# Kernel tuning notes

Measured on AMD Instinct MI355X. Metric: run time of the kernel, lower is better.

## Reference

```python
import jax, jax.numpy as jnp
import numpy as np

B, T, F, E = 256, 256, 8, 128
H = 2 * E  # hidden_dim = 2*embedding_dim = 256
NL = 5     # num_layers per LSTM stack


def setup_inputs() -> dict:
    key = jax.random.key(0)
    ks = jax.random.split(key, 9)
    s1 = 1.0 / np.sqrt(H)
    s2 = 1.0 / np.sqrt(E)
    u = lambda k, shape, s: jax.random.uniform(k, shape, jnp.float32, -s, s)
    return {
        "x": jax.random.normal(ks[0], (B, T, F), jnp.float32),
        # stack 1: input F -> hidden H, 5 layers. b = b_ih + b_hh combined.
        "w_ih0_1": u(ks[1], (4 * H, F), s1),
        "w_ihr_1": u(ks[2], (NL - 1, 4 * H, H), s1),
        "w_hh_1": u(ks[3], (NL, 4 * H, H), s1),
        "b_1": u(ks[4], (NL, 4 * H), s1),
        # stack 2: input H -> hidden E, 5 layers
        "w_ih0_2": u(ks[5], (4 * E, H), s2),
        "w_ihr_2": u(ks[6], (NL - 1, 4 * E, E), s2),
        "w_hh_2": u(ks[7], (NL, 4 * E, E), s2),
        "b_2": u(ks[8], (NL, 4 * E), s2),
    }


def _lstm_layer(x, w_ih, w_hh, b):
    """x: [B,T,D] -> (outputs [B,T,Hd], final hidden [B,Hd]). PyTorch gate order i,f,g,o."""
    Hd = w_hh.shape[-1]
    # precompute input contribution for all timesteps (the big GEMM)
    xg = jnp.einsum('btd,gd->tbg', x, w_ih) + b  # [T,B,4Hd]
    h0 = jnp.zeros((x.shape[0], Hd), x.dtype)

    def step(carry, xt):
        h, c = carry
        g = xt + h @ w_hh.T
        i, f, gg, o = jnp.split(g, 4, axis=-1)
        c = jax.nn.sigmoid(f) * c + jax.nn.sigmoid(i) * jnp.tanh(gg)
        h = jax.nn.sigmoid(o) * jnp.tanh(c)
        return (h, c), h

    (h, _), hs = jax.lax.scan(step, (h0, h0), xg)
    return jnp.swapaxes(hs, 0, 1), h


def _stack(x, w_ih0, w_ihr, w_hh, b):
    y, h = _lstm_layer(x, w_ih0, w_hh[0], b[0])
    for l in range(1, w_hh.shape[0]):
        y, h = _lstm_layer(y, w_ihr[l - 1], w_hh[l], b[l])
    return y, h


def reference(x, w_ih0_1, w_ihr_1, w_hh_1, b_1, w_ih0_2, w_ihr_2, w_hh_2, b_2):
    x = x.reshape(x.shape[0], T, F)
    y, _ = _stack(x, w_ih0_1, w_ihr_1, w_hh_1, b_1)   # [B,T,H]
    _, h = _stack(y, w_ih0_2, w_ihr_2, w_hh_2, b_2)   # h: [B,E] last layer final hidden
    return h
```

## Files before the change

### kernel.cpp

```cpp
#include <hip/hip_runtime.h>
#include <math.h>

typedef unsigned short u16;
typedef unsigned int   u32;
typedef unsigned long long u64;
typedef __bf16 bf16x8 __attribute__((ext_vector_type(8)));
typedef float  f32x4  __attribute__((ext_vector_type(4)));

#define BB 256
#define TT 256
#define HD 256
#define ED 128
#define NSTEPS 265

#define H_U32   (10 * 2 * BB * HD)
#define CTR_OFF H_U32
#define CTR_U32 512
#define XP_OFF  (H_U32 + CTR_U32)
#define XP_U32  (BB * TT * 8)
#define WT_OFF  (XP_OFF + XP_U32)

__constant__ size_t g_woff[10] = {0ul,589824ul,1638400ul,2686976ul,3735552ul,
                                  4784128ul,5177344ul,5439488ul,5701632ul,5963776ul};
__constant__ int g_cb[11] = {0,73728,204800,335872,466944,598016,
                             647168,679936,712704,745472,778240};

__device__ __forceinline__ u16 f2bf_hi(float f) {
    u32 u = __float_as_uint(f);
    u32 r = (u + 0x7FFFu + ((u >> 16) & 1u)) >> 16;
    return (u16)r;
}
__device__ __forceinline__ float bf2f(u16 h) { return __uint_as_float(((u32)h) << 16); }
__device__ __forceinline__ float sigmoidf_(float v) { return 1.0f / (1.0f + expf(-v)); }

__global__ __launch_bounds__(256) void zero_state(u32* wsd) {
    const int n = XP_OFF;
    for (int i = blockIdx.x * blockDim.x + threadIdx.x; i < n; i += gridDim.x * blockDim.x)
        wsd[i] = 0u;
}

__global__ __launch_bounds__(256) void conv_x(const float* __restrict__ x, u32* __restrict__ wsd) {
    u32* xp = wsd + XP_OFF;
    for (int i = blockIdx.x * blockDim.x + threadIdx.x; i < XP_U32; i += gridDim.x * blockDim.x) {
        float v = x[i];
        u16 hi = f2bf_hi(v);
        u16 lo = f2bf_hi(v - bf2f(hi));
        xp[i] = (u32)hi | ((u32)lo << 16);
    }
}

__global__ __launch_bounds__(256) void conv_all(
    const float* __restrict__ w_ih0_1, const float* __restrict__ w_ihr_1,
    const float* __restrict__ w_hh_1,
    const float* __restrict__ w_ih0_2, const float* __restrict__ w_ihr_2,
    const float* __restrict__ w_hh_2,
    u32* __restrict__ wsd)
{
    __bf16* dst0 = (__bf16*)(wsd + WT_OFF);
    const int nch = 778240;
    for (int ci = blockIdx.x * blockDim.x + threadIdx.x; ci < nch;
         ci += gridDim.x * blockDim.x) {
        int l = 0;
        while (ci >= g_cb[l + 1]) ++l;
        int di = ci - g_cb[l];

        const int hd  = (l < 5) ? 256 : 128;
        const int din = (l == 0) ? 32 : ((l < 6) ? 256 : 128);
        const int xw  = (l == 0) ? 8 : din;
        const int Kp  = din + hd;
        const int nk  = Kp >> 5;

        const float *wih, *whh; int wihld, whhld;
        if (l == 0)      { wih = w_ih0_1;                                whh = w_hh_1;
                           wihld = 8;   whhld = 256; }
        else if (l < 5)  { wih = w_ihr_1 + (size_t)(l - 1) * 1024 * 256; whh = w_hh_1 + (size_t)l * 1024 * 256;
                           wihld = 256; whhld = 256; }
        else if (l == 5) { wih = w_ih0_2;                                whh = w_hh_2;
                           wihld = 256; whhld = 128; }
        else             { wih = w_ihr_2 + (size_t)(l - 6) * 512 * 128;  whh = w_hh_2 + (size_t)(l - 5) * 512 * 128;
                           wihld = 128; whhld = 128; }

        int lane = di & 63;
        int rem  = di >> 6;
        int kt   = rem % nk;
        int rem2 = rem / nk;
        int p    = rem2 & 1;
        int g    = (rem2 >> 1) & 3;
        int jt   = rem2 >> 3;
        int r15  = lane & 15, kq = lane >> 4;
        int row  = g * hd + jt * 16 + r15;

        bf16x8 o8;
        #pragma unroll
        for (int e = 0; e < 8; ++e) {
            int k = kt * 32 + kq * 8 + e;
            float v = 0.0f;
            if (k < xw) v = wih[(size_t)row * wihld + k];
            else if (k >= din && k < Kp) v = whh[(size_t)row * whhld + (k - din)];
            __bf16 h = (__bf16)v;
            o8[e] = p ? (__bf16)(v - (float)h) : h;
        }
        *(bf16x8*)(dst0 + g_woff[l] + (size_t)di * 8) = o8;
    }
}

__device__ __forceinline__ void unpack8(const uint4& a, const uint4& b, bf16x8& bh, bf16x8& bl) {
    union { u32 u[4]; bf16x8 v; } H, L;
    H.u[0] = (a.x & 0xFFFFu) | (a.y << 16);
    H.u[1] = (a.z & 0xFFFFu) | (a.w << 16);
    H.u[2] = (b.x & 0xFFFFu) | (b.y << 16);
    H.u[3] = (b.z & 0xFFFFu) | (b.w << 16);
    L.u[0] = (a.x >> 16) | (a.y & 0xFFFF0000u);
    L.u[1] = (a.z >> 16) | (a.w & 0xFFFF0000u);
    L.u[2] = (b.x >> 16) | (b.y & 0xFFFF0000u);
    L.u[3] = (b.z >> 16) | (b.w & 0xFFFF0000u);
    bh = H.v; bl = L.v;
}

template<int NKI, int NKT, bool ISL0>
__device__ void run_persist(int l, int bid, int xcd, int jt, int bt, int hd,
    const float* __restrict__ bias, u32* __restrict__ hbuf, u32* __restrict__ ctr,
    const u32* __restrict__ xp, float* __restrict__ out, const u16* __restrict__ A_sh)
{
    constexpr int DIN = NKI * 32;
    constexpr int RD  = (NKT < 8) ? NKT : 8;

    const int tid  = threadIdx.x;
    const int lane = tid & 63;
    const int wv   = tid >> 6;
    const int r15  = lane & 15;
    const int kq   = lane >> 4;
    const int brow = bt * 128 + wv * 16 + r15;
    const int j0   = jt * 16 + kq * 4;

    float bgr[4][4];
    #pragma unroll
    for (int g = 0; g < 4; ++g) {
        float4 v = *(const float4*)&bias[g * hd + j0];
        bgr[g][0] = v.x; bgr[g][1] = v.y; bgr[g][2] = v.z; bgr[g][3] = v.w;
    }

    int offH[4], offL[4];
    #pragma unroll
    for (int g = 0; g < 4; ++g) {
        offH[g] = (g * 2)     * NKT * 512 + lane * 8;
        offL[g] = (g * 2 + 1) * NKT * 512 + lane * 8;
    }

    float4 cv = make_float4(0.f, 0.f, 0.f, 0.f);
    const int lm = (l > 0) ? (l - 1) : 0;

    for (int w = 0; w < NSTEPS; ++w) {
        const int t = w - l;
        if (t >= 0 && t < TT) {
            const u32* hin   = hbuf + ((size_t)lm * 2 + (t & 1)) * (BB * HD);
            const u32* hprev = hbuf + ((size_t)l * 2 + ((t & 1) ^ 1)) * (BB * HD);
            u32*       hout  = hbuf + ((size_t)l * 2 + (t & 1)) * (BB * HD);

            auto ldB = [&](int kt, uint4& A, uint4& B) {
                if constexpr (ISL0) {
                    if (kt == 0) {
                        if (kq == 0) {
                            const uint4* p = (const uint4*)(xp + ((size_t)brow * TT + t) * 8);
                            A = p[0]; B = p[1];
                        } else { A = make_uint4(0,0,0,0); B = make_uint4(0,0,0,0); }
                    } else {
                        const u32* p = hprev + (size_t)brow * HD + (kt * 32 - 32) + kq * 8;
                        A = *(const uint4*)p; B = *(const uint4*)(p + 4);
                    }
                } else {
                    const int k0 = kt * 32 + kq * 8;
                    const u32* p = (kt < NKI) ? (hin + (size_t)brow * HD + k0)
                                              : (hprev + (size_t)brow * HD + (k0 - DIN));
                    A = *(const uint4*)p; B = *(const uint4*)(p + 4);
                }
            };

            f32x4 acc0 = {0.f,0.f,0.f,0.f}, acc1 = {0.f,0.f,0.f,0.f};
            f32x4 acc2 = {0.f,0.f,0.f,0.f}, acc3 = {0.f,0.f,0.f,0.f};

            uint4 rA[RD], rB[RD];
            #pragma unroll
            for (int i = 0; i < RD; ++i) ldB(i, rA[i], rB[i]);

            #pragma unroll
            for (int kt = 0; kt < NKT; ++kt) {
                bf16x8 bh, bl;
                unpack8(rA[kt % RD], rB[kt % RD], bh, bl);
                if (kt + RD < NKT) ldB(kt + RD, rA[kt % RD], rB[kt % RD]);

                const int kof = kt * 512;
                bf16x8 a0h = *(const bf16x8*)&A_sh[offH[0] + kof];
                bf16x8 a1h = *(const bf16x8*)&A_sh[offH[1] + kof];
                bf16x8 a2h = *(const bf16x8*)&A_sh[offH[2] + kof];
                bf16x8 a3h = *(const bf16x8*)&A_sh[offH[3] + kof];
                bf16x8 a0l = *(const bf16x8*)&A_sh[offL[0] + kof];
                bf16x8 a1l = *(const bf16x8*)&A_sh[offL[1] + kof];
                bf16x8 a2l = *(const bf16x8*)&A_sh[offL[2] + kof];
                bf16x8 a3l = *(const bf16x8*)&A_sh[offL[3] + kof];

                acc0 = __builtin_amdgcn_mfma_f32_16x16x32_bf16(a0h, bh, acc0, 0, 0, 0);
                acc1 = __builtin_amdgcn_mfma_f32_16x16x32_bf16(a1h, bh, acc1, 0, 0, 0);
                acc2 = __builtin_amdgcn_mfma_f32_16x16x32_bf16(a2h, bh, acc2, 0, 0, 0);
                acc3 = __builtin_amdgcn_mfma_f32_16x16x32_bf16(a3h, bh, acc3, 0, 0, 0);
                acc0 = __builtin_amdgcn_mfma_f32_16x16x32_bf16(a0h, bl, acc0, 0, 0, 0);
                acc1 = __builtin_amdgcn_mfma_f32_16x16x32_bf16(a1h, bl, acc1, 0, 0, 0);
                acc2 = __builtin_amdgcn_mfma_f32_16x16x32_bf16(a2h, bl, acc2, 0, 0, 0);
                acc3 = __builtin_amdgcn_mfma_f32_16x16x32_bf16(a3h, bl, acc3, 0, 0, 0);
                acc0 = __builtin_amdgcn_mfma_f32_16x16x32_bf16(a0l, bh, acc0, 0, 0, 0);
                acc1 = __builtin_amdgcn_mfma_f32_16x16x32_bf16(a1l, bh, acc1, 0, 0, 0);
                acc2 = __builtin_amdgcn_mfma_f32_16x16x32_bf16(a2l, bh, acc2, 0, 0, 0);
                acc3 = __builtin_amdgcn_mfma_f32_16x16x32_bf16(a3l, bh, acc3, 0, 0, 0);
            }

            float4 hv;
            {
                float i_, f_, g_, o_;
                i_ = sigmoidf_(acc0[0] + bgr[0][0]); f_ = sigmoidf_(acc1[0] + bgr[1][0]);
                g_ = tanhf   (acc2[0] + bgr[2][0]); o_ = sigmoidf_(acc3[0] + bgr[3][0]);
                cv.x = fmaf(f_, cv.x, i_ * g_); hv.x = o_ * tanhf(cv.x);
                i_ = sigmoidf_(acc0[1] + bgr[0][1]); f_ = sigmoidf_(acc1[1] + bgr[1][1]);
                g_ = tanhf   (acc2[1] + bgr[2][1]); o_ = sigmoidf_(acc3[1] + bgr[3][1]);
                cv.y = fmaf(f_, cv.y, i_ * g_); hv.y = o_ * tanhf(cv.y);
                i_ = sigmoidf_(acc0[2] + bgr[0][2]); f_ = sigmoidf_(acc1[2] + bgr[1][2]);
                g_ = tanhf   (acc2[2] + bgr[2][2]); o_ = sigmoidf_(acc3[2] + bgr[3][2]);
                cv.z = fmaf(f_, cv.z, i_ * g_); hv.z = o_ * tanhf(cv.z);
                i_ = sigmoidf_(acc0[3] + bgr[0][3]); f_ = sigmoidf_(acc1[3] + bgr[1][3]);
                g_ = tanhf   (acc2[3] + bgr[2][3]); o_ = sigmoidf_(acc3[3] + bgr[3][3]);
                cv.w = fmaf(f_, cv.w, i_ * g_); hv.w = o_ * tanhf(cv.w);
            }

            u32 pk0, pk1, pk2, pk3;
            {
                u16 h0 = f2bf_hi(hv.x); pk0 = (u32)h0 | ((u32)f2bf_hi(hv.x - bf2f(h0)) << 16);
                u16 h1 = f2bf_hi(hv.y); pk1 = (u32)h1 | ((u32)f2bf_hi(hv.y - bf2f(h1)) << 16);
                u16 h2 = f2bf_hi(hv.z); pk2 = (u32)h2 | ((u32)f2bf_hi(hv.z - bf2f(h2)) << 16);
                u16 h3 = f2bf_hi(hv.w); pk3 = (u32)h3 | ((u32)f2bf_hi(hv.w - bf2f(h3)) << 16);
            }
            u64* hp = (u64*)(hout + (size_t)brow * HD + j0);
            __hip_atomic_store(hp + 0, (u64)pk0 | ((u64)pk1 << 32), __ATOMIC_RELAXED, __HIP_MEMORY_SCOPE_AGENT);
            __hip_atomic_store(hp + 1, (u64)pk2 | ((u64)pk3 << 32), __ATOMIC_RELAXED, __HIP_MEMORY_SCOPE_AGENT);

            if (l == 9 && t == TT - 1)
                *(float4*)&out[(size_t)brow * ED + j0] = hv;
        }

        __syncthreads();
        if (tid == 0) {
            __hip_atomic_fetch_add(&ctr[xcd * 32], 1u,
                                   __ATOMIC_RELAXED, __HIP_MEMORY_SCOPE_AGENT);
            const u32 w1 = (u32)(w + 1);
            if (bid == 0) {
                for (int it = 0; it < (1 << 22); ++it) {
                    bool ok = true;
                    #pragma unroll
                    for (int r = 0; r < 8; ++r) {
                        u32 tgt = ((r == 7) ? 16u : 32u) * w1;
                        ok &= (__hip_atomic_load(&ctr[r * 32], __ATOMIC_RELAXED,
                                                 __HIP_MEMORY_SCOPE_AGENT) >= tgt);
                    }
                    if (ok) break;
                    __builtin_amdgcn_s_sleep(1);
                }
                __hip_atomic_store(&ctr[256], w1, __ATOMIC_RELAXED, __HIP_MEMORY_SCOPE_AGENT);
            } else {
                for (int it = 0; it < (1 << 22); ++it) {
                    if (__hip_atomic_load(&ctr[256], __ATOMIC_RELAXED,
                                          __HIP_MEMORY_SCOPE_AGENT) >= w1) break;
                    __builtin_amdgcn_s_sleep(1);
                }
            }
            __builtin_amdgcn_fence(__ATOMIC_ACQUIRE, "agent");
        }
        __syncthreads();
    }
}

__global__ __launch_bounds__(512, 2) void lstm_persist(
    const float* __restrict__ b_1, const float* __restrict__ b_2,
    u32* __restrict__ wsd, float* __restrict__ out)
{
    __shared__ __align__(16) u16 A_sh[65536];

    const int bid = blockIdx.x;
    const int xcd = bid & 7, slot = bid >> 3;
    int l, jt, bt;
    if (xcd < 5)      { l = xcd;               bt = slot >> 4;        jt = slot & 15; }
    else if (xcd == 5){ l = 5 + (slot >> 4);   bt = (slot >> 3) & 1;  jt = slot & 7; }
    else if (xcd == 6){ l = 7 + (slot >> 4);   bt = (slot >> 3) & 1;  jt = slot & 7; }
    else              { if (slot >= 16) return; l = 9; bt = slot >> 3; jt = slot & 7; }

    const int hd  = (l < 5) ? 256 : 128;
    const int din = (l == 0) ? 32 : ((l < 6) ? 256 : 128);
    const int nk  = (din + hd) >> 5;
    const float* bias = (l < 5) ? (b_1 + l * 1024) : (b_2 + (l - 5) * 512);

    u32* hbuf = wsd;
    u32* ctr  = wsd + CTR_OFF;
    const u32* xp = wsd + XP_OFF;
    const u16* wt = (const u16*)(wsd + WT_OFF);

    {
        const uint4* src = (const uint4*)(wt + g_woff[l] + (size_t)jt * 8 * nk * 512);
        uint4* dst = (uint4*)A_sh;
        const int n4 = nk * 512;
        for (int i = threadIdx.x; i < n4; i += 512) dst[i] = src[i];
    }
    __syncthreads();

    if (l == 0)
        run_persist<1, 9, true >(l, bid, xcd, jt, bt, hd, bias, hbuf, ctr, xp, out, A_sh);
    else if (l < 5)
        run_persist<8, 16, false>(l, bid, xcd, jt, bt, hd, bias, hbuf, ctr, xp, out, A_sh);
    else if (l == 5)
        run_persist<8, 12, false>(l, bid, xcd, jt, bt, hd, bias, hbuf, ctr, xp, out, A_sh);
    else
        run_persist<4, 8, false>(l, bid, xcd, jt, bt, hd, bias, hbuf, ctr, xp, out, A_sh);
}

extern "C" void kernel_launch(void* const* d_in, const int* in_sizes, int n_in,
                              void* d_out, int out_size, void* d_ws, size_t ws_size,
                              hipStream_t stream) {
    const float* x       = (const float*)d_in[0];
    const float* w_ih0_1 = (const float*)d_in[1];
    const float* w_ihr_1 = (const float*)d_in[2];
    const float* w_hh_1  = (const float*)d_in[3];
    const float* b_1     = (const float*)d_in[4];
    const float* w_ih0_2 = (const float*)d_in[5];
    const float* w_ihr_2 = (const float*)d_in[6];
    const float* w_hh_2  = (const float*)d_in[7];
    const float* b_2     = (const float*)d_in[8];
    u32*   wsd = (u32*)d_ws;
    float* out = (float*)d_out;

    hipLaunchKernelGGL(zero_state, dim3(1024), dim3(256), 0, stream, wsd);
    hipLaunchKernelGGL(conv_all, dim3(1024), dim3(256), 0, stream,
                       w_ih0_1, w_ihr_1, w_hh_1, w_ih0_2, w_ihr_2, w_hh_2, wsd);
    hipLaunchKernelGGL(conv_x, dim3(256), dim3(256), 0, stream, x, wsd);
    hipLaunchKernelGGL(lstm_persist, dim3(256), dim3(512), 0, stream,
                       b_1, b_2, wsd, out);
}
```

Baseline: 3.286 ms.

## Switch recurrent GEMM to 32x32x16 MFMA with gate-interleaved weight layout

Replaces the four 16x16x32 MFMA accumulators per wave with a single 32x32x16 MFMA accumulator, where the 32 output rows interleave the four gates across 8 hidden units. The weight pre-pack and the LDS slice layout are reorganised to match, and waves are split by batch group and hidden half. This cuts LDS A-fragment loads per MFMA and uses the larger MFMA shape, but doubles the K-step count and changes how often the h buffer is loaded, which may raise latency on the serial recurrence path.

Result: slower. 5.104 ms (+55.3%).

```diff
diff --git a/kernel.cpp b/kernel.cpp
--- a/kernel.cpp
+++ b/kernel.cpp
@@ -5,7 +5,7 @@
 typedef unsigned int   u32;
 typedef unsigned long long u64;
 typedef __bf16 bf16x8 __attribute__((ext_vector_type(8)));
-typedef float  f32x4  __attribute__((ext_vector_type(4)));
+typedef float  f32x16 __attribute__((ext_vector_type(16)));
 
 #define BB 256
 #define TT 256
@@ -68,7 +68,7 @@
         const int din = (l == 0) ? 32 : ((l < 6) ? 256 : 128);
         const int xw  = (l == 0) ? 8 : din;
         const int Kp  = din + hd;
-        const int nk  = Kp >> 5;
+        const int NK2 = Kp >> 4;
 
         const float *wih, *whh; int wihld, whhld;
         if (l == 0)      { wih = w_ih0_1;                                whh = w_hh_1;
@@ -82,18 +82,20 @@
 
         int lane = di & 63;
         int rem  = di >> 6;
-        int kt   = rem % nk;
-        int rem2 = rem / nk;
+        int s    = rem % NK2;
+        int rem2 = rem / NK2;
         int p    = rem2 & 1;
-        int g    = (rem2 >> 1) & 3;
-        int jt   = rem2 >> 3;
-        int r15  = lane & 15, kq = lane >> 4;
-        int row  = g * hd + jt * 16 + r15;
+        int jh   = (rem2 >> 1) & 1;
+        int jt   = rem2 >> 2;
+        int r31  = lane & 31;
+        int gate = r31 >> 3, jl = r31 & 7;
+        int kh   = (lane >> 5) * 8;
+        int row  = gate * hd + jt * 16 + jh * 8 + jl;
 
         bf16x8 o8;
         #pragma unroll
         for (int e = 0; e < 8; ++e) {
-            int k = kt * 32 + kq * 8 + e;
+            int k = s * 16 + kh + e;
             float v = 0.0f;
             if (k < xw) v = wih[(size_t)row * wihld + k];
             else if (k >= din && k < Kp) v = whh[(size_t)row * whhld + (k - din)];
@@ -122,29 +124,28 @@
     const float* __restrict__ bias, u32* __restrict__ hbuf, u32* __restrict__ ctr,
     const u32* __restrict__ xp, float* __restrict__ out, const u16* __restrict__ A_sh)
 {
+    constexpr int NK2 = NKT * 2;
     constexpr int DIN = NKI * 32;
-    constexpr int RD  = (NKT < 8) ? NKT : 8;
-
-    const int tid  = threadIdx.x;
-    const int lane = tid & 63;
-    const int wv   = tid >> 6;
-    const int r15  = lane & 15;
-    const int kq   = lane >> 4;
-    const int brow = bt * 128 + wv * 16 + r15;
-    const int j0   = jt * 16 + kq * 4;
-
-    float bgr[4][4];
+    constexpr int RS  = (NK2 < 8) ? NK2 : 8;
+
+    const int tid   = threadIdx.x;
+    const int lane  = tid & 63;
+    const int wv    = tid >> 6;
+    const int bg    = wv >> 1;
+    const int jh    = wv & 1;
+    const int r31   = lane & 31;
+    const int kh    = (lane >> 5) * 8;
+    const int b     = bt * 128 + bg * 32 + r31;
+    const int jbase = jt * 16 + jh * 8 + (lane >> 5) * 4;
+
+    const int hiBase = ((jh * 2 + 0) * NK2) * 512 + lane * 8;
+    const int loBase = ((jh * 2 + 1) * NK2) * 512 + lane * 8;
+
+    float bias_r[4][4];
     #pragma unroll
     for (int g = 0; g < 4; ++g) {
-        float4 v = *(const float4*)&bias[g * hd + j0];
-        bgr[g][0] = v.x; bgr[g][1] = v.y; bgr[g][2] = v.z; bgr[g][3] = v.w;
-    }
-
-    int offH[4], offL[4];
-    #pragma unroll
-    for (int g = 0; g < 4; ++g) {
-        offH[g] = (g * 2)     * NKT * 512 + lane * 8;
-        offL[g] = (g * 2 + 1) * NKT * 512 + lane * 8;
+        float4 v = *(const float4*)&bias[g * hd + jbase];
+        bias_r[g][0] = v.x; bias_r[g][1] = v.y; bias_r[g][2] = v.z; bias_r[g][3] = v.w;
     }
 
     float4 cv = make_float4(0.f, 0.f, 0.f, 0.f);
@@ -157,76 +158,63 @@
             const u32* hprev = hbuf + ((size_t)l * 2 + ((t & 1) ^ 1)) * (BB * HD);
             u32*       hout  = hbuf + ((size_t)l * 2 + (t & 1)) * (BB * HD);
 
-            auto ldB = [&](int kt, uint4& A, uint4& B) {
+            auto ldB = [&](int s, uint4& qa, uint4& qb) {
                 if constexpr (ISL0) {
-                    if (kt == 0) {
-                        if (kq == 0) {
-                            const uint4* p = (const uint4*)(xp + ((size_t)brow * TT + t) * 8);
-                            A = p[0]; B = p[1];
-                        } else { A = make_uint4(0,0,0,0); B = make_uint4(0,0,0,0); }
+                    if (s == 0) {
+                        if (lane < 32) {
+                            const uint4* p = (const uint4*)(xp + ((size_t)b * TT + t) * 8);
+                            qa = p[0]; qb = p[1];
+                        } else { qa = make_uint4(0,0,0,0); qb = make_uint4(0,0,0,0); }
+                    } else if (s == 1) {
+                        qa = make_uint4(0,0,0,0); qb = make_uint4(0,0,0,0);
                     } else {
-                        const u32* p = hprev + (size_t)brow * HD + (kt * 32 - 32) + kq * 8;
-                        A = *(const uint4*)p; B = *(const uint4*)(p + 4);
+                        const u32* p = hprev + (size_t)b * HD + (s * 16 + kh - 32);
+                        qa = *(const uint4*)p; qb = *(const uint4*)(p + 4);
                     }
                 } else {
-                    const int k0 = kt * 32 + kq * 8;
-                    const u32* p = (kt < NKI) ? (hin + (size_t)brow * HD + k0)
-                                              : (hprev + (size_t)brow * HD + (k0 - DIN));
-                    A = *(const uint4*)p; B = *(const uint4*)(p + 4);
+                    const int k0 = s * 16 + kh;
+                    const u32* p = (k0 < DIN) ? (hin + (size_t)b * HD + k0)
+                                              : (hprev + (size_t)b * HD + (k0 - DIN));
+                    qa = *(const uint4*)p; qb = *(const uint4*)(p + 4);
                 }
             };
 
-            f32x4 acc0 = {0.f,0.f,0.f,0.f}, acc1 = {0.f,0.f,0.f,0.f};
-            f32x4 acc2 = {0.f,0.f,0.f,0.f}, acc3 = {0.f,0.f,0.f,0.f};
-
-            uint4 rA[RD], rB[RD];
+            f32x16 acc;
             #pragma unroll
-            for (int i = 0; i < RD; ++i) ldB(i, rA[i], rB[i]);
-
+            for (int i = 0; i < 16; ++i) acc[i] = 0.f;
+
+            uint4 ra[RS], rb[RS];
             #pragma unroll
-            for (int kt = 0; kt < NKT; ++kt) {
+            for (int i = 0; i < RS; ++i) ldB(i, ra[i], rb[i]);
+
+            #pragma unroll
+            for (int s = 0; s < NK2; ++s) {
                 bf16x8 bh, bl;
-                unpack8(rA[kt % RD], rB[kt % RD], bh, bl);
-                if (kt + RD < NKT) ldB(kt + RD, rA[kt % RD], rB[kt % RD]);
-
-                const int kof = kt * 512;
-                bf16x8 a0h = *(const bf16x8*)&A_sh[offH[0] + kof];
-                bf16x8 a1h = *(const bf16x8*)&A_sh[offH[1] + kof];
-                bf16x8 a2h = *(const bf16x8*)&A_sh[offH[2] + kof];
-                bf16x8 a3h = *(const bf16x8*)&A_sh[offH[3] + kof];
-                bf16x8 a0l = *(const bf16x8*)&A_sh[offL[0] + kof];
-                bf16x8 a1l = *(const bf16x8*)&A_sh[offL[1] + kof];
-                bf16x8 a2l = *(const bf16x8*)&A_sh[offL[2] + kof];
-                bf16x8 a3l = *(const bf16x8*)&A_sh[offL[3] + kof];
-
-                acc0 = __builtin_amdgcn_mfma_f32_16x16x32_bf16(a0h, bh, acc0, 0, 0, 0);
-                acc1 = __builtin_amdgcn_mfma_f32_16x16x32_bf16(a1h, bh, acc1, 0, 0, 0);
-                acc2 = __builtin_amdgcn_mfma_f32_16x16x32_bf16(a2h, bh, acc2, 0, 0, 0);
-                acc3 = __builtin_amdgcn_mfma_f32_16x16x32_bf16(a3h, bh, acc3, 0, 0, 0);
-                acc0 = __builtin_amdgcn_mfma_f32_16x16x32_bf16(a0h, bl, acc0, 0, 0, 0);
-                acc1 = __builtin_amdgcn_mfma_f32_16x16x32_bf16(a1h, bl, acc1, 0, 0, 0);
-                acc2 = __builtin_amdgcn_mfma_f32_16x16x32_bf16(a2h, bl, acc2, 0, 0, 0);
-                acc3 = __builtin_amdgcn_mfma_f32_16x16x32_bf16(a3h, bl, acc3, 0, 0, 0);
-                acc0 = __builtin_amdgcn_mfma_f32_16x16x32_bf16(a0l, bh, acc0, 0, 0, 0);
-                acc1 = __builtin_amdgcn_mfma_f32_16x16x32_bf16(a1l, bh, acc1, 0, 0, 0);
-                acc2 = __builtin_amdgcn_mfma_f32_16x16x32_bf16(a2l, bh, acc2, 0, 0, 0);
-                acc3 = __builtin_amdgcn_mfma_f32_16x16x32_bf16(a3l, bh, acc3, 0, 0, 0);
+                unpack8(ra[s % RS], rb[s % RS], bh, bl);
+                if (s + RS < NK2) ldB(s + RS, ra[s % RS], rb[s % RS]);
+
+                bf16x8 ah = *(const bf16x8*)&A_sh[hiBase + s * 512];
+                bf16x8 al = *(const bf16x8*)&A_sh[loBase + s * 512];
+
+                acc = __builtin_amdgcn_mfma_f32_32x32x16_bf16(ah, bh, acc, 0, 0, 0);
+                acc = __builtin_amdgcn_mfma_f32_32x32x16_bf16(ah, bl, acc, 0, 0, 0);
+                acc = __builtin_amdgcn_mfma_f32_32x32x16_bf16(al, bh, acc, 0, 0, 0);
             }
 
             float4 hv;
             {
                 float i_, f_, g_, o_;
-                i_ = sigmoidf_(acc0[0] + bgr[0][0]); f_ = sigmoidf_(acc1[0] + bgr[1][0]);
-                g_ = tanhf   (acc2[0] + bgr[2][0]); o_ = sigmoidf_(acc3[0] + bgr[3][0]);
+                i_ = sigmoidf_(acc[0]  + bias_r[0][0]); f_ = sigmoidf_(acc[4]  + bias_r[1][0]);
+                g_ = tanhf   (acc[8]  + bias_r[2][0]); o_ = sigmoidf_(acc[12] + bias_r[3][0]);
                 cv.x = fmaf(f_, cv.x, i_ * g_); hv.x = o_ * tanhf(cv.x);
-                i_ = sigmoidf_(acc0[1] + bgr[0][1]); f_ = sigmoidf_(acc1[1] + bgr[1][1]);
-                g_ = tanhf   (acc2[1] + bgr[2][1]); o_ = sigmoidf_(acc3[1] + bgr[3][1]);
+                i_ = sigmoidf_(acc[1]  + bias_r[0][1]); f_ = sigmoidf_(acc[5]  + bias_r[1][1]);
+                g_ = tanhf   (acc[9]  + bias_r[2][1]); o_ = sigmoidf_(acc[13] + bias_r[3][1]);
                 cv.y = fmaf(f_, cv.y, i_ * g_); hv.y = o_ * tanhf(cv.y);
-                i_ = sigmoidf_(acc0[2] + bgr[0][2]); f_ = sigmoidf_(acc1[2] + bgr[1][2]);
-                g_ = tanhf   (acc2[2] + bgr[2][2]); o_ = sigmoidf_(acc3[2] + bgr[3][2]);
+                i_ = sigmoidf_(acc[2]  + bias_r[0][2]); f_ = sigmoidf_(acc[6]  + bias_r[1][2]);
+                g_ = tanhf   (acc[10] + bias_r[2][2]); o_ = sigmoidf_(acc[14] + bias_r[3][2]);
                 cv.z = fmaf(f_, cv.z, i_ * g_); hv.z = o_ * tanhf(cv.z);
-                i_ = sigmoidf_(acc0[3] + bgr[0][3]); f_ = sigmoidf_(acc1[3] + bgr[1][3]);
-                g_ = tanhf   (acc2[3] + bgr[2][3]); o_ = sigmoidf_(acc3[3] + bgr[3][3]);
+                i_ = sigmoidf_(acc[3]  + bias_r[0][3]); f_ = sigmoidf_(acc[7]  + bias_r[1][3]);
+                g_ = tanhf   (acc[11] + bias_r[2][3]); o_ = sigmoidf_(acc[15] + bias_r[3][3]);
                 cv.w = fmaf(f_, cv.w, i_ * g_); hv.w = o_ * tanhf(cv.w);
             }
 
@@ -237,12 +225,12 @@
                 u16 h2 = f2bf_hi(hv.z); pk2 = (u32)h2 | ((u32)f2bf_hi(hv.z - bf2f(h2)) << 16);
                 u16 h3 = f2bf_hi(hv.w); pk3 = (u32)h3 | ((u32)f2bf_hi(hv.w - bf2f(h3)) << 16);
             }
-            u64* hp = (u64*)(hout + (size_t)brow * HD + j0);
+            u64* hp = (u64*)(hout + (size_t)b * HD + jbase);
             __hip_atomic_store(hp + 0, (u64)pk0 | ((u64)pk1 << 32), __ATOMIC_RELAXED, __HIP_MEMORY_SCOPE_AGENT);
             __hip_atomic_store(hp + 1, (u64)pk2 | ((u64)pk3 << 32), __ATOMIC_RELAXED, __HIP_MEMORY_SCOPE_AGENT);
 
             if (l == 9 && t == TT - 1)
-                *(float4*)&out[(size_t)brow * ED + j0] = hv;
+                *(float4*)&out[(size_t)b * ED + jbase] = hv;
         }
 
         __syncthreads();
@@ -292,7 +280,7 @@
 
     const int hd  = (l < 5) ? 256 : 128;
     const int din = (l == 0) ? 32 : ((l < 6) ? 256 : 128);
-    const int nk  = (din + hd) >> 5;
+    const int NK2 = (din + hd) >> 4;
     const float* bias = (l < 5) ? (b_1 + l * 1024) : (b_2 + (l - 5) * 512);
 
     u32* hbuf = wsd;
@@ -301,9 +289,9 @@
     const u16* wt = (const u16*)(wsd + WT_OFF);
 
     {
-        const uint4* src = (const uint4*)(wt + g_woff[l] + (size_t)jt * 8 * nk * 512);
+        const uint4* src = (const uint4*)(wt + g_woff[l] + (size_t)jt * 4 * NK2 * 512);
         uint4* dst = (uint4*)A_sh;
-        const int n4 = nk * 512;
+        const int n4 = NK2 * 256;
         for (int i = threadIdx.x; i < n4; i += 512) dst[i] = src[i];
     }
     __syncthreads();
```

## Retile LSTM step MFMA to 2x2 per-wave tiles with gate-interleaved weight rows

Applied to the files above, without the earlier changes.

Weight rows are re-laid out so each 16-row MFMA tile interleaves the four gates for four hidden units. Each wave now computes a 2x2 block: two weight tiles (hidden halves) by two batch tiles. This halves the LDS weight-fragment reads per MFMA and lets the gate nonlinearities run lane-locally from one accumulator. In exchange, each wave loads two batch rows of h, the prefetch depth drops from 8 to 4, and output stores become scattered 32-bit atomics instead of 64-bit vector stores.

After: 5.194 ms. 58.1% more time.

```diff
diff --git a/kernel.cpp b/kernel.cpp
--- a/kernel.cpp
+++ b/kernel.cpp
@@ -85,15 +85,17 @@
         int kt   = rem % nk;
         int rem2 = rem / nk;
         int p    = rem2 & 1;
-        int g    = (rem2 >> 1) & 3;
+        int mt   = (rem2 >> 1) & 1;
+        int jh   = (rem2 >> 2) & 1;
         int jt   = rem2 >> 3;
-        int r15  = lane & 15, kq = lane >> 4;
-        int row  = g * hd + jt * 16 + r15;
+        int r15  = lane & 15, kqc = lane >> 4;
+        int jloc = r15 >> 2, gate = r15 & 3;
+        int row  = gate * hd + jt * 16 + jh * 8 + mt * 4 + jloc;
 
         bf16x8 o8;
         #pragma unroll
         for (int e = 0; e < 8; ++e) {
-            int k = kt * 32 + kq * 8 + e;
+            int k = kt * 32 + kqc * 8 + e;
             float v = 0.0f;
             if (k < xw) v = wih[(size_t)row * wihld + k];
             else if (k >= din && k < Kp) v = whh[(size_t)row * whhld + (k - din)];
@@ -123,31 +125,31 @@
     const u32* __restrict__ xp, float* __restrict__ out, const u16* __restrict__ A_sh)
 {
     constexpr int DIN = NKI * 32;
-    constexpr int RD  = (NKT < 8) ? NKT : 8;
+    constexpr int RS  = (NKT < 4) ? NKT : 4;
 
     const int tid  = threadIdx.x;
     const int lane = tid & 63;
     const int wv   = tid >> 6;
+    const int bq   = wv >> 1;
+    const int jh   = wv & 1;
     const int r15  = lane & 15;
-    const int kq   = lane >> 4;
-    const int brow = bt * 128 + wv * 16 + r15;
-    const int j0   = jt * 16 + kq * 4;
-
-    float bgr[4][4];
+    const int kqc  = lane >> 4;
+    const int b0r  = bt * 128 + bq * 32 + r15;
+    const int jm0  = jt * 16 + jh * 8 + kqc;
+
+    const int hiB0 = ((jh * 4 + 0) * NKT) * 512 + lane * 8;
+    const int loB0 = ((jh * 4 + 1) * NKT) * 512 + lane * 8;
+    const int hiB1 = ((jh * 4 + 2) * NKT) * 512 + lane * 8;
+    const int loB1 = ((jh * 4 + 3) * NKT) * 512 + lane * 8;
+
+    float bias_r[2][4];
     #pragma unroll
-    for (int g = 0; g < 4; ++g) {
-        float4 v = *(const float4*)&bias[g * hd + j0];
-        bgr[g][0] = v.x; bgr[g][1] = v.y; bgr[g][2] = v.z; bgr[g][3] = v.w;
-    }
-
-    int offH[4], offL[4];
-    #pragma unroll
-    for (int g = 0; g < 4; ++g) {
-        offH[g] = (g * 2)     * NKT * 512 + lane * 8;
-        offL[g] = (g * 2 + 1) * NKT * 512 + lane * 8;
-    }
-
-    float4 cv = make_float4(0.f, 0.f, 0.f, 0.f);
+    for (int mt = 0; mt < 2; ++mt)
+        #pragma unroll
+        for (int g = 0; g < 4; ++g)
+            bias_r[mt][g] = bias[g * hd + jm0 + mt * 4];
+
+    f32x4 cv = {0.f, 0.f, 0.f, 0.f};
     const int lm = (l > 0) ? (l - 1) : 0;
 
     for (int w = 0; w < NSTEPS; ++w) {
@@ -157,92 +159,89 @@
             const u32* hprev = hbuf + ((size_t)l * 2 + ((t & 1) ^ 1)) * (BB * HD);
             u32*       hout  = hbuf + ((size_t)l * 2 + (t & 1)) * (BB * HD);
 
-            auto ldB = [&](int kt, uint4& A, uint4& B) {
+            auto ldB = [&](int kt, uint4& a0, uint4& b0q, uint4& a1, uint4& b1q) {
                 if constexpr (ISL0) {
                     if (kt == 0) {
-                        if (kq == 0) {
-                            const uint4* p = (const uint4*)(xp + ((size_t)brow * TT + t) * 8);
-                            A = p[0]; B = p[1];
-                        } else { A = make_uint4(0,0,0,0); B = make_uint4(0,0,0,0); }
+                        if (kqc == 0) {
+                            const uint4* p0 = (const uint4*)(xp + ((size_t)b0r * TT + t) * 8);
+                            const uint4* p1 = (const uint4*)(xp + ((size_t)(b0r + 16) * TT + t) * 8);
+                            a0 = p0[0]; b0q = p0[1]; a1 = p1[0]; b1q = p1[1];
+                        } else {
+                            a0 = make_uint4(0,0,0,0); b0q = a0; a1 = a0; b1q = a0;
+                        }
                     } else {
-                        const u32* p = hprev + (size_t)brow * HD + (kt * 32 - 32) + kq * 8;
-                        A = *(const uint4*)p; B = *(const uint4*)(p + 4);
+                        const int k0 = kt * 32 - 32 + kqc * 8;
+                        const u32* p0 = hprev + (size_t)b0r * HD + k0;
+                        const u32* p1 = hprev + (size_t)(b0r + 16) * HD + k0;
+                        a0 = *(const uint4*)p0; b0q = *(const uint4*)(p0 + 4);
+                        a1 = *(const uint4*)p1; b1q = *(const uint4*)(p1 + 4);
                     }
                 } else {
-                    const int k0 = kt * 32 + kq * 8;
-                    const u32* p = (kt < NKI) ? (hin + (size_t)brow * HD + k0)
-                                              : (hprev + (size_t)brow * HD + (k0 - DIN));
-                    A = *(const uint4*)p; B = *(const uint4*)(p + 4);
+                    const int k0 = kt * 32 + kqc * 8;
+                    const u32* base = (k0 < DIN) ? hin : hprev;
+                    const int ko = (k0 < DIN) ? k0 : (k0 - DIN);
+                    const u32* p0 = base + (size_t)b0r * HD + ko;
+                    const u32* p1 = base + (size_t)(b0r + 16) * HD + ko;
+                    a0 = *(const uint4*)p0; b0q = *(const uint4*)(p0 + 4);
+                    a1 = *(const uint4*)p1; b1q = *(const uint4*)(p1 + 4);
                 }
             };
 
-            f32x4 acc0 = {0.f,0.f,0.f,0.f}, acc1 = {0.f,0.f,0.f,0.f};
-            f32x4 acc2 = {0.f,0.f,0.f,0.f}, acc3 = {0.f,0.f,0.f,0.f};
-
-            uint4 rA[RD], rB[RD];
+            f32x4 acc00 = {0.f,0.f,0.f,0.f}, acc01 = {0.f,0.f,0.f,0.f};
+            f32x4 acc10 = {0.f,0.f,0.f,0.f}, acc11 = {0.f,0.f,0.f,0.f};
+
+            uint4 ra0[RS], rb0[RS], ra1[RS], rb1[RS];
             #pragma unroll
-            for (int i = 0; i < RD; ++i) ldB(i, rA[i], rB[i]);
+            for (int i = 0; i < RS; ++i) ldB(i, ra0[i], rb0[i], ra1[i], rb1[i]);
 
             #pragma unroll
             for (int kt = 0; kt < NKT; ++kt) {
-                bf16x8 bh, bl;
-                unpack8(rA[kt % RD], rB[kt % RD], bh, bl);
-                if (kt + RD < NKT) ldB(kt + RD, rA[kt % RD], rB[kt % RD]);
+                bf16x8 bh0, bl0, bh1, bl1;
+                unpack8(ra0[kt % RS], rb0[kt % RS], bh0, bl0);
+                unpack8(ra1[kt % RS], rb1[kt % RS], bh1, bl1);
+                if (kt + RS < NKT)
+                    ldB(kt + RS, ra0[kt % RS], rb0[kt % RS], ra1[kt % RS], rb1[kt % RS]);
 
                 const int kof = kt * 512;
-                bf16x8 a0h = *(const bf16x8*)&A_sh[offH[0] + kof];
-                bf16x8 a1h = *(const bf16x8*)&A_sh[offH[1] + kof];
-                bf16x8 a2h = *(const bf16x8*)&A_sh[offH[2] + kof];
-                bf16x8 a3h = *(const bf16x8*)&A_sh[offH[3] + kof];
-                bf16x8 a0l = *(const bf16x8*)&A_sh[offL[0] + kof];
-                bf16x8 a1l = *(const bf16x8*)&A_sh[offL[1] + kof];
-                bf16x8 a2l = *(const bf16x8*)&A_sh[offL[2] + kof];
-                bf16x8 a3l = *(const bf16x8*)&A_sh[offL[3] + kof];
-
-                acc0 = __builtin_amdgcn_mfma_f32_16x16x32_bf16(a0h, bh, acc0, 0, 0, 0);
-                acc1 = __builtin_amdgcn_mfma_f32_16x16x32_bf16(a1h, bh, acc1, 0, 0, 0);
-                acc2 = __builtin_amdgcn_mfma_f32_16x16x32_bf16(a2h, bh, acc2, 0, 0, 0);
-                acc3 = __builtin_amdgcn_mfma_f32_16x16x32_bf16(a3h, bh, acc3, 0, 0, 0);
-                acc0 = __builtin_amdgcn_mfma_f32_16x16x32_bf16(a0h, bl, acc0, 0, 0, 0);
-                acc1 = __builtin_amdgcn_mfma_f32_16x16x32_bf16(a1h, bl, acc1, 0, 0, 0);
-                acc2 = __builtin_amdgcn_mfma_f32_16x16x32_bf16(a2h, bl, acc2, 0, 0, 0);
-                acc3 = __builtin_amdgcn_mfma_f32_16x16x32_bf16(a3h, bl, acc3, 0, 0, 0);
-                acc0 = __builtin_amdgcn_mfma_f32_16x16x32_bf16(a0l, bh, acc0, 0, 0, 0);
-                acc1 = __builtin_amdgcn_mfma_f32_16x16x32_bf16(a1l, bh, acc1, 0, 0, 0);
-                acc2 = __builtin_amdgcn_mfma_f32_16x16x32_bf16(a2l, bh, acc2, 0, 0, 0);
-                acc3 = __builtin_amdgcn_mfma_f32_16x16x32_bf16(a3l, bh, acc3, 0, 0, 0);
+                bf16x8 a0h = *(const bf16x8*)&A_sh[hiB0 + kof];
+                bf16x8 a0l = *(const bf16x8*)&A_sh[loB0 + kof];
+                bf16x8 a1h = *(const bf16x8*)&A_sh[hiB1 + kof];
+                bf16x8 a1l = *(const bf16x8*)&A_sh[loB1 + kof];
+
+                acc00 = __builtin_amdgcn_mfma_f32_16x16x32_bf16(a0h, bh0, acc00, 0, 0, 0);
+                acc01 = __builtin_amdgcn_mfma_f32_16x16x32_bf16(a0h, bh1, acc01, 0, 0, 0);
+                acc10 = __builtin_amdgcn_mfma_f32_16x16x32_bf16(a1h, bh0, acc10, 0, 0, 0);
+                acc11 = __builtin_amdgcn_mfma_f32_16x16x32_bf16(a1h, bh1, acc11, 0, 0, 0);
+                acc00 = __builtin_amdgcn_mfma_f32_16x16x32_bf16(a0h, bl0, acc00, 0, 0, 0);
+                acc01 = __builtin_amdgcn_mfma_f32_16x16x32_bf16(a0h, bl1, acc01, 0, 0, 0);
+                acc10 = __builtin_amdgcn_mfma_f32_16x16x32_bf16(a1h, bl0, acc10, 0, 0, 0);
+                acc11 = __builtin_amdgcn_mfma_f32_16x16x32_bf16(a1h, bl1, acc11, 0, 0, 0);
+                acc00 = __builtin_amdgcn_mfma_f32_16x16x32_bf16(a0l, bh0, acc00, 0, 0, 0);
+                acc01 = __builtin_amdgcn_mfma_f32_16x16x32_bf16(a0l, bh1, acc01, 0, 0, 0);
+                acc10 = __builtin_amdgcn_mfma_f32_16x16x32_bf16(a1l, bh0, acc10, 0, 0, 0);
+                acc11 = __builtin_amdgcn_mfma_f32_16x16x32_bf16(a1l, bh1, acc11, 0, 0, 0);
             }
 
-            float4 hv;
-            {
-                float i_, f_, g_, o_;
-                i_ = sigmoidf_(acc0[0] + bgr[0][0]); f_ = sigmoidf_(acc1[0] + bgr[1][0]);
-                g_ = tanhf   (acc2[0] + bgr[2][0]); o_ = sigmoidf_(acc3[0] + bgr[3][0]);
-                cv.x = fmaf(f_, cv.x, i_ * g_); hv.x = o_ * tanhf(cv.x);
-                i_ = sigmoidf_(acc0[1] + bgr[0][1]); f_ = sigmoidf_(acc1[1] + bgr[1][1]);
-                g_ = tanhf   (acc2[1] + bgr[2][1]); o_ = sigmoidf_(acc3[1] + bgr[3][1]);
-                cv.y = fmaf(f_, cv.y, i_ * g_); hv.y = o_ * tanhf(cv.y);
-                i_ = sigmoidf_(acc0[2] + bgr[0][2]); f_ = sigmoidf_(acc1[2] + bgr[1][2]);
-                g_ = tanhf   (acc2[2] + bgr[2][2]); o_ = sigmoidf_(acc3[2] + bgr[3][2]);
-                cv.z = fmaf(f_, cv.z, i_ * g_); hv.z = o_ * tanhf(cv.z);
-                i_ = sigmoidf_(acc0[3] + bgr[0][3]); f_ = sigmoidf_(acc1[3] + bgr[1][3]);
-                g_ = tanhf   (acc2[3] + bgr[2][3]); o_ = sigmoidf_(acc3[3] + bgr[3][3]);
-                cv.w = fmaf(f_, cv.w, i_ * g_); hv.w = o_ * tanhf(cv.w);
+            #pragma unroll
+            for (int mt = 0; mt < 2; ++mt) {
+                #pragma unroll
+                for (int nt = 0; nt < 2; ++nt) {
+                    const f32x4& ac = mt ? (nt ? acc11 : acc10) : (nt ? acc01 : acc00);
+                    const int ci = mt * 2 + nt;
+                    float i_ = sigmoidf_(ac[0] + bias_r[mt][0]);
+                    float f_ = sigmoidf_(ac[1] + bias_r[mt][1]);
+                    float g_ = tanhf   (ac[2] + bias_r[mt][2]);
+                    float o_ = sigmoidf_(ac[3] + bias_r[mt][3]);
+                    cv[ci] = fmaf(f_, cv[ci], i_ * g_);
+                    float hv = o_ * tanhf(cv[ci]);
+                    u16 h0 = f2bf_hi(hv);
+                    u32 pk = (u32)h0 | ((u32)f2bf_hi(hv - bf2f(h0)) << 16);
+                    const int b = b0r + nt * 16, j = jm0 + mt * 4;
+                    __hip_atomic_store(hout + (size_t)b * HD + j, pk,
+                                       __ATOMIC_RELAXED, __HIP_MEMORY_SCOPE_AGENT);
+                    if (l == 9 && t == TT - 1) out[(size_t)b * ED + j] = hv;
+                }
             }
-
-            u32 pk0, pk1, pk2, pk3;
-            {
-                u16 h0 = f2bf_hi(hv.x); pk0 = (u32)h0 | ((u32)f2bf_hi(hv.x - bf2f(h0)) << 16);
-                u16 h1 = f2bf_hi(hv.y); pk1 = (u32)h1 | ((u32)f2bf_hi(hv.y - bf2f(h1)) << 16);
-                u16 h2 = f2bf_hi(hv.z); pk2 = (u32)h2 | ((u32)f2bf_hi(hv.z - bf2f(h2)) << 16);
-                u16 h3 = f2bf_hi(hv.w); pk3 = (u32)h3 | ((u32)f2bf_hi(hv.w - bf2f(h3)) << 16);
-            }
-            u64* hp = (u64*)(hout + (size_t)brow * HD + j0);
-            __hip_atomic_store(hp + 0, (u64)pk0 | ((u64)pk1 << 32), __ATOMIC_RELAXED, __HIP_MEMORY_SCOPE_AGENT);
-            __hip_atomic_store(hp + 1, (u64)pk2 | ((u64)pk3 << 32), __ATOMIC_RELAXED, __HIP_MEMORY_SCOPE_AGENT);
-
-            if (l == 9 && t == TT - 1)
-                *(float4*)&out[(size_t)brow * ED + j0] = hv;
         }
 
         __syncthreads();
```

## Halve per-block hidden tile and double persistent grid with interleaved gate layout

Applied to the files above, without the earlier changes.

Each block now computes 8 hidden units instead of 16, with the four gates packed into two MFMA tiles by interleaving gate rows in the weight layout. The grid doubles to 512 blocks, shared memory per block halves, and occupancy is raised to 4 blocks per CU, with a new layer-to-XCD assignment. The goal is to shorten per-step critical-path latency in the wavefront-pipelined recurrence by spreading the work over more CUs. The cost is more blocks taking part in each cross-block barrier step, and the barrier targets change accordingly.

Measured after the change: 5.216 ms. 1.59x slower.

```diff
diff --git a/kernel.cpp b/kernel.cpp
--- a/kernel.cpp
+++ b/kernel.cpp
@@ -85,15 +85,16 @@
         int kt   = rem % nk;
         int rem2 = rem / nk;
         int p    = rem2 & 1;
-        int g    = (rem2 >> 1) & 3;
-        int jt   = rem2 >> 3;
-        int r15  = lane & 15, kq = lane >> 4;
-        int row  = g * hd + jt * 16 + r15;
+        int mt   = (rem2 >> 1) & 1;
+        int jt   = rem2 >> 2;
+        int r15  = lane & 15, kqc = lane >> 4;
+        int jloc = r15 >> 1, gp = r15 & 1;
+        int row  = (mt * 2 + gp) * hd + jt * 8 + jloc;
 
         bf16x8 o8;
         #pragma unroll
         for (int e = 0; e < 8; ++e) {
-            int k = kt * 32 + kq * 8 + e;
+            int k = kt * 32 + kqc * 8 + e;
             float v = 0.0f;
             if (k < xw) v = wih[(size_t)row * wihld + k];
             else if (k >= din && k < Kp) v = whh[(size_t)row * whhld + (k - din)];
@@ -118,36 +119,32 @@
 }
 
 template<int NKI, int NKT, bool ISL0>
-__device__ void run_persist(int l, int bid, int xcd, int jt, int bt, int hd,
+__device__ void run_persist(int l, int bid, int xcd, int jt, int bt, int hd, u32 arr7,
     const float* __restrict__ bias, u32* __restrict__ hbuf, u32* __restrict__ ctr,
     const u32* __restrict__ xp, float* __restrict__ out, const u16* __restrict__ A_sh)
 {
     constexpr int DIN = NKI * 32;
-    constexpr int RD  = (NKT < 8) ? NKT : 8;
+    constexpr int RS  = (NKT < 4) ? NKT : 4;
 
     const int tid  = threadIdx.x;
     const int lane = tid & 63;
     const int wv   = tid >> 6;
     const int r15  = lane & 15;
-    const int kq   = lane >> 4;
+    const int kqc  = lane >> 4;
     const int brow = bt * 128 + wv * 16 + r15;
-    const int j0   = jt * 16 + kq * 4;
-
-    float bgr[4][4];
-    #pragma unroll
-    for (int g = 0; g < 4; ++g) {
-        float4 v = *(const float4*)&bias[g * hd + j0];
-        bgr[g][0] = v.x; bgr[g][1] = v.y; bgr[g][2] = v.z; bgr[g][3] = v.w;
-    }
-
-    int offH[4], offL[4];
-    #pragma unroll
-    for (int g = 0; g < 4; ++g) {
-        offH[g] = (g * 2)     * NKT * 512 + lane * 8;
-        offL[g] = (g * 2 + 1) * NKT * 512 + lane * 8;
-    }
-
-    float4 cv = make_float4(0.f, 0.f, 0.f, 0.f);
+    const int jA   = jt * 8 + kqc * 2;
+
+    const int t0h = (0 * NKT) * 512 + lane * 8;
+    const int t0l = (1 * NKT) * 512 + lane * 8;
+    const int t1h = (2 * NKT) * 512 + lane * 8;
+    const int t1l = (3 * NKT) * 512 + lane * 8;
+
+    float2 bI = *(const float2*)&bias[0 * hd + jA];
+    float2 bF = *(const float2*)&bias[1 * hd + jA];
+    float2 bG = *(const float2*)&bias[2 * hd + jA];
+    float2 bO = *(const float2*)&bias[3 * hd + jA];
+
+    float cA = 0.f, cB = 0.f;
     const int lm = (l > 0) ? (l - 1) : 0;
 
     for (int w = 0; w < NSTEPS; ++w) {
@@ -160,89 +157,71 @@
             auto ldB = [&](int kt, uint4& A, uint4& B) {
                 if constexpr (ISL0) {
                     if (kt == 0) {
-                        if (kq == 0) {
+                        if (kqc == 0) {
                             const uint4* p = (const uint4*)(xp + ((size_t)brow * TT + t) * 8);
                             A = p[0]; B = p[1];
                         } else { A = make_uint4(0,0,0,0); B = make_uint4(0,0,0,0); }
                     } else {
-                        const u32* p = hprev + (size_t)brow * HD + (kt * 32 - 32) + kq * 8;
+                        const u32* p = hprev + (size_t)brow * HD + (kt * 32 - 32) + kqc * 8;
                         A = *(const uint4*)p; B = *(const uint4*)(p + 4);
                     }
                 } else {
-                    const int k0 = kt * 32 + kq * 8;
-                    const u32* p = (kt < NKI) ? (hin + (size_t)brow * HD + k0)
+                    const int k0 = kt * 32 + kqc * 8;
+                    const u32* p = (k0 < DIN) ? (hin + (size_t)brow * HD + k0)
                                               : (hprev + (size_t)brow * HD + (k0 - DIN));
                     A = *(const uint4*)p; B = *(const uint4*)(p + 4);
                 }
             };
 
-            f32x4 acc0 = {0.f,0.f,0.f,0.f}, acc1 = {0.f,0.f,0.f,0.f};
-            f32x4 acc2 = {0.f,0.f,0.f,0.f}, acc3 = {0.f,0.f,0.f,0.f};
-
-            uint4 rA[RD], rB[RD];
+            f32x4 acc0 = {0.f,0.f,0.f,0.f};
+            f32x4 acc1 = {0.f,0.f,0.f,0.f};
+
+            uint4 ra[RS], rb[RS];
             #pragma unroll
-            for (int i = 0; i < RD; ++i) ldB(i, rA[i], rB[i]);
+            for (int i = 0; i < RS; ++i) ldB(i, ra[i], rb[i]);
 
             #pragma unroll
             for (int kt = 0; kt < NKT; ++kt) {
                 bf16x8 bh, bl;
-                unpack8(rA[kt % RD], rB[kt % RD], bh, bl);
-                if (kt + RD < NKT) ldB(kt + RD, rA[kt % RD], rB[kt % RD]);
+                unpack8(ra[kt % RS], rb[kt % RS], bh, bl);
+                if (kt + RS < NKT) ldB(kt + RS, ra[kt % RS], rb[kt % RS]);
 
                 const int kof = kt * 512;
-                bf16x8 a0h = *(const bf16x8*)&A_sh[offH[0] + kof];
-                bf16x8 a1h = *(const bf16x8*)&A_sh[offH[1] + kof];
-                bf16x8 a2h = *(const bf16x8*)&A_sh[offH[2] + kof];
-                bf16x8 a3h = *(const bf16x8*)&A_sh[offH[3] + kof];
-                bf16x8 a0l = *(const bf16x8*)&A_sh[offL[0] + kof];
-                bf16x8 a1l = *(const bf16x8*)&A_sh[offL[1] + kof];
-                bf16x8 a2l = *(const bf16x8*)&A_sh[offL[2] + kof];
-                bf16x8 a3l = *(const bf16x8*)&A_sh[offL[3] + kof];
+                bf16x8 a0h = *(const bf16x8*)&A_sh[t0h + kof];
+                bf16x8 a0l = *(const bf16x8*)&A_sh[t0l + kof];
+                bf16x8 a1h = *(const bf16x8*)&A_sh[t1h + kof];
+                bf16x8 a1l = *(const bf16x8*)&A_sh[t1l + kof];
 
                 acc0 = __builtin_amdgcn_mfma_f32_16x16x32_bf16(a0h, bh, acc0, 0, 0, 0);
                 acc1 = __builtin_amdgcn_mfma_f32_16x16x32_bf16(a1h, bh, acc1, 0, 0, 0);
-                acc2 = __builtin_amdgcn_mfma_f32_16x16x32_bf16(a2h, bh, acc2, 0, 0, 0);
-                acc3 = __builtin_amdgcn_mfma_f32_16x16x32_bf16(a3h, bh, acc3, 0, 0, 0);
                 acc0 = __builtin_amdgcn_mfma_f32_16x16x32_bf16(a0h, bl, acc0, 0, 0, 0);
                 acc1 = __builtin_amdgcn_mfma_f32_16x16x32_bf16(a1h, bl, acc1, 0, 0, 0);
-                acc2 = __builtin_amdgcn_mfma_f32_16x16x32_bf16(a2h, bl, acc2, 0, 0, 0);
-                acc3 = __builtin_amdgcn_mfma_f32_16x16x32_bf16(a3h, bl, acc3, 0, 0, 0);
                 acc0 = __builtin_amdgcn_mfma_f32_16x16x32_bf16(a0l, bh, acc0, 0, 0, 0);
                 acc1 = __builtin_amdgcn_mfma_f32_16x16x32_bf16(a1l, bh, acc1, 0, 0, 0);
-                acc2 = __builtin_amdgcn_mfma_f32_16x16x32_bf16(a2l, bh, acc2, 0, 0, 0);
-                acc3 = __builtin_amdgcn_mfma_f32_16x16x32_bf16(a3l, bh, acc3, 0, 0, 0);
             }
 
-            float4 hv;
+            float hA, hB;
             {
                 float i_, f_, g_, o_;
-                i_ = sigmoidf_(acc0[0] + bgr[0][0]); f_ = sigmoidf_(acc1[0] + bgr[1][0]);
-                g_ = tanhf   (acc2[0] + bgr[2][0]); o_ = sigmoidf_(acc3[0] + bgr[3][0]);
-                cv.x = fmaf(f_, cv.x, i_ * g_); hv.x = o_ * tanhf(cv.x);
-                i_ = sigmoidf_(acc0[1] + bgr[0][1]); f_ = sigmoidf_(acc1[1] + bgr[1][1]);
-                g_ = tanhf   (acc2[1] + bgr[2][1]); o_ = sigmoidf_(acc3[1] + bgr[3][1]);
-                cv.y = fmaf(f_, cv.y, i_ * g_); hv.y = o_ * tanhf(cv.y);
-                i_ = sigmoidf_(acc0[2] + bgr[0][2]); f_ = sigmoidf_(acc1[2] + bgr[1][2]);
-                g_ = tanhf   (acc2[2] + bgr[2][2]); o_ = sigmoidf_(acc3[2] + bgr[3][2]);
-                cv.z = fmaf(f_, cv.z, i_ * g_); hv.z = o_ * tanhf(cv.z);
-                i_ = sigmoidf_(acc0[3] + bgr[0][3]); f_ = sigmoidf_(acc1[3] + bgr[1][3]);
-                g_ = tanhf   (acc2[3] + bgr[2][3]); o_ = sigmoidf_(acc3[3] + bgr[3][3]);
-                cv.w = fmaf(f_, cv.w, i_ * g_); hv.w = o_ * tanhf(cv.w);
+                i_ = sigmoidf_(acc0[0] + bI.x); f_ = sigmoidf_(acc0[1] + bF.x);
+                g_ = tanhf   (acc1[0] + bG.x); o_ = sigmoidf_(acc1[1] + bO.x);
+                cA = fmaf(f_, cA, i_ * g_); hA = o_ * tanhf(cA);
+                i_ = sigmoidf_(acc0[2] + bI.y); f_ = sigmoidf_(acc0[3] + bF.y);
+                g_ = tanhf   (acc1[2] + bG.y); o_ = sigmoidf_(acc1[3] + bO.y);
+                cB = fmaf(f_, cB, i_ * g_); hB = o_ * tanhf(cB);
             }
 
-            u32 pk0, pk1, pk2, pk3;
+            u32 pkA, pkB;
             {
-                u16 h0 = f2bf_hi(hv.x); pk0 = (u32)h0 | ((u32)f2bf_hi(hv.x - bf2f(h0)) << 16);
-                u16 h1 = f2bf_hi(hv.y); pk1 = (u32)h1 | ((u32)f2bf_hi(hv.y - bf2f(h1)) << 16);
-                u16 h2 = f2bf_hi(hv.z); pk2 = (u32)h2 | ((u32)f2bf_hi(hv.z - bf2f(h2)) << 16);
-                u16 h3 = f2bf_hi(hv.w); pk3 = (u32)h3 | ((u32)f2bf_hi(hv.w - bf2f(h3)) << 16);
+                u16 h0 = f2bf_hi(hA); pkA = (u32)h0 | ((u32)f2bf_hi(hA - bf2f(h0)) << 16);
+                u16 h1 = f2bf_hi(hB); pkB = (u32)h1 | ((u32)f2bf_hi(hB - bf2f(h1)) << 16);
             }
-            u64* hp = (u64*)(hout + (size_t)brow * HD + j0);
-            __hip_atomic_store(hp + 0, (u64)pk0 | ((u64)pk1 << 32), __ATOMIC_RELAXED, __HIP_MEMORY_SCOPE_AGENT);
-            __hip_atomic_store(hp + 1, (u64)pk2 | ((u64)pk3 << 32), __ATOMIC_RELAXED, __HIP_MEMORY_SCOPE_AGENT);
+            __hip_atomic_store((u64*)(hout + (size_t)brow * HD + jA),
+                               (u64)pkA | ((u64)pkB << 32),
+                               __ATOMIC_RELAXED, __HIP_MEMORY_SCOPE_AGENT);
 
             if (l == 9 && t == TT - 1)
-                *(float4*)&out[(size_t)brow * ED + j0] = hv;
+                *(float2*)&out[(size_t)brow * ED + jA] = make_float2(hA, hB);
         }
 
         __syncthreads();
@@ -255,7 +234,7 @@
                     bool ok = true;
                     #pragma unroll
                     for (int r = 0; r < 8; ++r) {
-                        u32 tgt = ((r == 7) ? 16u : 32u) * w1;
+                        u32 tgt = ((r == 7) ? arr7 : 64u) * w1;
                         ok &= (__hip_atomic_load(&ctr[r * 32], __ATOMIC_RELAXED,
                                                  __HIP_MEMORY_SCOPE_AGENT) >= tgt);
                     }
@@ -276,19 +255,31 @@
     }
 }
 
-__global__ __launch_bounds__(512, 2) void lstm_persist(
+__global__ __launch_bounds__(512, 4) void lstm_persist(
     const float* __restrict__ b_1, const float* __restrict__ b_2,
     u32* __restrict__ wsd, float* __restrict__ out)
 {
-    __shared__ __align__(16) u16 A_sh[65536];
+    __shared__ __align__(16) u16 A_sh[32768];
 
     const int bid = blockIdx.x;
     const int xcd = bid & 7, slot = bid >> 3;
     int l, jt, bt;
-    if (xcd < 5)      { l = xcd;               bt = slot >> 4;        jt = slot & 15; }
-    else if (xcd == 5){ l = 5 + (slot >> 4);   bt = (slot >> 3) & 1;  jt = slot & 7; }
-    else if (xcd == 6){ l = 7 + (slot >> 4);   bt = (slot >> 3) & 1;  jt = slot & 7; }
-    else              { if (slot >= 16) return; l = 9; bt = slot >> 3; jt = slot & 7; }
+    if (xcd < 2)       { bt = xcd;
+                         if (slot < 32)      { l = 0; jt = slot; }
+                         else if (slot < 48) { l = 5; jt = slot - 32; }
+                         else                { l = 6; jt = slot - 48; } }
+    else if (xcd < 4)  { bt = xcd - 2;
+                         if (slot < 32)      { l = 1; jt = slot; }
+                         else if (slot < 48) { l = 7; jt = slot - 32; }
+                         else                { l = 8; jt = slot - 48; } }
+    else if (xcd == 4) { if (slot < 32)      { l = 2; bt = 0; jt = slot; }
+                         else if (slot < 48) { l = 9; bt = 0; jt = slot - 32; }
+                         else                { l = 9; bt = 1; jt = slot - 48; } }
+    else if (xcd == 5) { if (slot < 32)      { l = 2; bt = 1; jt = slot; }
+                         else                { l = 3; bt = 0; jt = slot - 32; } }
+    else if (xcd == 6) { if (slot < 32)      { l = 3; bt = 1; jt = slot; }
+                         else                { l = 4; bt = 0; jt = slot - 32; } }
+    else               { if (slot >= 32) return; l = 4; bt = 1; jt = slot; }
 
     const int hd  = (l < 5) ? 256 : 128;
     const int din = (l == 0) ? 32 : ((l < 6) ? 256 : 128);
@@ -301,21 +292,21 @@
     const u16* wt = (const u16*)(wsd + WT_OFF);
 
     {
-        const uint4* src = (const uint4*)(wt + g_woff[l] + (size_t)jt * 8 * nk * 512);
+        const uint4* src = (const uint4*)(wt + g_woff[l] + (size_t)jt * 4 * nk * 512);
         uint4* dst = (uint4*)A_sh;
-        const int n4 = nk * 512;
+        const int n4 = nk * 256;
         for (int i = threadIdx.x; i < n4; i += 512) dst[i] = src[i];
     }
     __syncthreads();
 
     if (l == 0)
-        run_persist<1, 9, true >(l, bid, xcd, jt, bt, hd, bias, hbuf, ctr, xp, out, A_sh);
+        run_persist<1, 9, true >(l, bid, xcd, jt, bt, hd, 32u, bias, hbuf, ctr, xp, out, A_sh);
     else if (l < 5)
-        run_persist<8, 16, false>(l, bid, xcd, jt, bt, hd, bias, hbuf, ctr, xp, out, A_sh);
+        run_persist<8, 16, false>(l, bid, xcd, jt, bt, hd, 32u, bias, hbuf, ctr, xp, out, A_sh);
     else if (l == 5)
-        run_persist<8, 12, false>(l, bid, xcd, jt, bt, hd, bias, hbuf, ctr, xp, out, A_sh);
+        run_persist<8, 12, false>(l, bid, xcd, jt, bt, hd, 32u, bias, hbuf, ctr, xp, out, A_sh);
     else
-        run_persist<4, 8, false>(l, bid, xcd, jt, bt, hd, bias, hbuf, ctr, xp, out, A_sh);
+        run_persist<4, 8, false>(l, bid, xcd, jt, bt, hd, 32u, bias, hbuf, ctr, xp, out, A_sh);
 }
 
 extern "C" void kernel_launch(void* const* d_in, const int* in_sizes, int n_in,
@@ -337,6 +328,6 @@
     hipLaunchKernelGGL(conv_all, dim3(1024), dim3(256), 0, stream,
                        w_ih0_1, w_ihr_1, w_hh_1, w_ih0_2, w_ihr_2, w_hh_2, wsd);
     hipLaunchKernelGGL(conv_x, dim3(256), dim3(256), 0, stream, x, wsd);
-    hipLaunchKernelGGL(lstm_persist, dim3(256), dim3(512), 0, stream,
+    hipLaunchKernelGGL(lstm_persist, dim3(512), dim3(512), 0, stream,
                        b_1, b_2, wsd, out);
 }
```
